# Performance work log

Hardware: AMD Instinct MI355X
Metric: run time of the kernel (lower is better)

Reference implementation:

```python
import jax, jax.numpy as jnp
import numpy as np

BS, S, D, H = 2, 2048, 1024, 16
DH = D // H  # 64


def setup_inputs() -> dict:
    key = jax.random.key(0)
    k1, k2, k3 = jax.random.split(key, 3)
    x = jax.random.normal(k1, (BS, S, D), dtype=jnp.float32)
    w_qkv = jax.random.normal(k2, (D, H, 3 * DH), dtype=jnp.float32) * (D ** -0.5)
    b_qkv = jnp.zeros((H, 3 * DH), dtype=jnp.float32)
    w_out = jax.random.normal(k3, (H, DH, D), dtype=jnp.float32) * (D ** -0.5)
    b_out = jnp.zeros((D,), dtype=jnp.float32)
    return {"x": x, "w_qkv": w_qkv, "b_qkv": b_qkv, "w_out": w_out, "b_out": b_out}


def reference(x, w_qkv, b_qkv, w_out, b_out):
    dtype = x.dtype
    # QKV projection: DenseGeneral(features=(H, 3*DH)) -> [B, S, H, 3*DH]
    qkv = jnp.einsum("bsd,dhf->bshf", x, w_qkv) + b_qkv
    q, k, v = jnp.split(qkv, 3, axis=-1)  # each [B, S, H, DH]

    scale = DH ** -0.5
    q = (q * scale).astype(jnp.float32)
    k = k.astype(jnp.float32)
    # Full causal attention with fp32 scores (as in original)
    weights = jnp.einsum("bqhd,bkhd->bhqk", q, k)  # [B, H, S, S]
    causal = jnp.tril(jnp.ones((S, S), dtype=bool))[None, None, :, :]
    weights = jnp.where(causal, weights, jnp.finfo(jnp.float32).min)
    weights = jax.nn.softmax(weights, axis=-1).astype(dtype)
    attn = jnp.einsum("bhqk,bkhd->bqhd", weights, v).astype(dtype)

    # Output projection: DenseGeneral(D, axis=(-2, -1))
    out = jnp.einsum("bqhd,hdo->bqo", attn, w_out) + b_out
    return out
```

## Files before the change

### kernel.cpp

```cpp
#include <hip/hip_runtime.h>
#include <hip/hip_bf16.h>
#include <stdint.h>

#define NBS 2
#define SEQ 2048
#define DMODEL 1024
#define NH 16
#define DHEAD 64
#define MROWS (NBS*SEQ)
#define NQKV (NH*3*DHEAD)

typedef __bf16 bf16;
typedef __bf16 bf16x8 __attribute__((ext_vector_type(8)));
typedef float f32x4 __attribute__((ext_vector_type(4)));

#define LOG2E 1.44269504088896f

static __device__ __forceinline__ void gload_lds16(const bf16* g, bf16* l) {
    __builtin_amdgcn_global_load_lds(
        (const __attribute__((address_space(1))) uint32_t*)g,
        (__attribute__((address_space(3))) uint32_t*)l, 16, 0, 0);
}

static __device__ __forceinline__ bf16x8 ld_b8(const bf16* p) {
    return __builtin_bit_cast(bf16x8, *(const uint4*)p);
}


__global__ void k_cvt(const float* __restrict__ in, bf16* __restrict__ out, int n4) {
    int i = blockIdx.x * blockDim.x + threadIdx.x;
    if (i < n4) {
        float4 v = ((const float4*)in)[i];
        ushort4 o;
        o.x = __builtin_bit_cast(unsigned short, (bf16)v.x);
        o.y = __builtin_bit_cast(unsigned short, (bf16)v.y);
        o.z = __builtin_bit_cast(unsigned short, (bf16)v.z);
        o.w = __builtin_bit_cast(unsigned short, (bf16)v.w);
        ((ushort4*)out)[i] = o;
    }
}

__global__ void k_tcvt(const float* __restrict__ in, bf16* __restrict__ out, int R, int C) {
    __shared__ float t[32][33];
    int tx = threadIdx.x, ty = threadIdx.y;
    int r0 = blockIdx.y * 32, c0 = blockIdx.x * 32;
#pragma unroll
    for (int i = 0; i < 4; i++)
        t[ty + i*8][tx] = in[(size_t)(r0 + ty + i*8) * C + (c0 + tx)];
    __syncthreads();
#pragma unroll
    for (int i = 0; i < 4; i++)
        out[(size_t)(c0 + ty + i*8) * R + (r0 + tx)] = (bf16)t[tx][ty + i*8];
}

template<int KD>
static __device__ __forceinline__ void gemm_tile(
        const bf16* __restrict__ A, const bf16* __restrict__ Bt,
        bf16* As, bf16* Bs, f32x4 acc[4][4], int tile_m, int tile_n) {
    int tid = threadIdx.x;
    int wave = tid >> 6, lane = tid & 63;
    int wr = wave >> 1, wc = wave & 1;
    int g = lane >> 4, r = lane & 15;
    int srow = lane >> 2, schunk = (lane & 3) * 8;

#pragma unroll
    for (int m = 0; m < 4; m++)
#pragma unroll
        for (int n = 0; n < 4; n++)
            acc[m][n] = (f32x4){0.f, 0.f, 0.f, 0.f};

    for (int k0 = 0; k0 < KD; k0 += 32) {
#pragma unroll
        for (int i = 0; i < 2; i++) {
            int ii = wave + i * 4;
            gload_lds16(A  + (size_t)(tile_m + ii*16 + srow) * KD + k0 + schunk, As + ii*512);
            gload_lds16(Bt + (size_t)(tile_n + ii*16 + srow) * KD + k0 + schunk, Bs + ii*512);
        }
        __syncthreads();
        bf16x8 af[4], bfr[4];
#pragma unroll
        for (int m = 0; m < 4; m++) af[m]  = *(const bf16x8*)(As + (wr*64 + m*16 + r)*32 + g*8);
#pragma unroll
        for (int n = 0; n < 4; n++) bfr[n] = *(const bf16x8*)(Bs + (wc*64 + n*16 + r)*32 + g*8);
#pragma unroll
        for (int m = 0; m < 4; m++)
#pragma unroll
            for (int n = 0; n < 4; n++)
                acc[m][n] = __builtin_amdgcn_mfma_f32_16x16x32_bf16(af[m], bfr[n], acc[m][n], 0, 0, 0);
        __syncthreads();
    }
}

__global__ __launch_bounds__(256) void k_gemm_qkv(
        const bf16* __restrict__ A, const bf16* __restrict__ Bt,
        const float* __restrict__ bias,
        bf16* __restrict__ Q, bf16* __restrict__ Kp, bf16* __restrict__ Vp) {
    __shared__ __align__(16) bf16 As[128*32];
    __shared__ __align__(16) bf16 Bs[128*32];
    f32x4 acc[4][4];
    int tile_m = blockIdx.y * 128, tile_n = blockIdx.x * 128;
    gemm_tile<DMODEL>(A, Bt, As, Bs, acc, tile_m, tile_n);

    int wave = threadIdx.x >> 6, lane = threadIdx.x & 63;
    int wr = wave >> 1, wc = wave & 1, g = lane >> 4, r = lane & 15;
#pragma unroll
    for (int m = 0; m < 4; m++) {
#pragma unroll
        for (int n = 0; n < 4; n++) {
            int col = tile_n + wc*64 + n*16 + r;
            int h = col / 192, f = col % 192;
            int kind = f >> 6, d = f & 63;
            float bv = bias[col];
#pragma unroll
            for (int j = 0; j < 4; j++) {
                int row = tile_m + wr*64 + m*16 + g*4 + j;
                int b = row >> 11, s = row & 2047;
                float v = acc[m][n][j] + bv;
                size_t addr = (((size_t)(b*NH + h)) * SEQ + s) * DHEAD + d;
                if (kind == 0)      Q[addr]  = (bf16)(v * 0.125f);
                else if (kind == 1) Kp[addr] = (bf16)v;
                else                Vp[addr] = (bf16)v;
            }
        }
    }
}

__global__ __launch_bounds__(256) void k_gemm_out(
        const bf16* __restrict__ A, const bf16* __restrict__ Bt,
        const float* __restrict__ bias, float* __restrict__ out) {
    __shared__ __align__(16) bf16 As[128*32];
    __shared__ __align__(16) bf16 Bs[128*32];
    f32x4 acc[4][4];
    int tile_m = blockIdx.y * 128, tile_n = blockIdx.x * 128;
    gemm_tile<DMODEL>(A, Bt, As, Bs, acc, tile_m, tile_n);

    int wave = threadIdx.x >> 6, lane = threadIdx.x & 63;
    int wr = wave >> 1, wc = wave & 1, g = lane >> 4, r = lane & 15;
#pragma unroll
    for (int m = 0; m < 4; m++) {
#pragma unroll
        for (int n = 0; n < 4; n++) {
            int col = tile_n + wc*64 + n*16 + r;
            float bv = bias[col];
#pragma unroll
            for (int j = 0; j < 4; j++) {
                int row = tile_m + wr*64 + m*16 + g*4 + j;
                out[(size_t)row * DMODEL + col] = acc[m][n][j] + bv;
            }
        }
    }
}

#define QBLK 128
#define KVB 64

__global__ __launch_bounds__(256) void k_attn(
        const bf16* __restrict__ Q, const bf16* __restrict__ K,
        const bf16* __restrict__ V, bf16* __restrict__ O) {
    int bh = blockIdx.y;
    int qc = (bh >= 16) ? (15 - blockIdx.x) : blockIdx.x;
    int q0 = qc * QBLK;
    int tid = threadIdx.x, wave = tid >> 6, lane = tid & 63;
    int g = lane >> 4, r = lane & 15;

    __shared__ __align__(16) bf16 Ks[2][KVB*72];
    __shared__ __align__(16) bf16 VsT[2][KVB*72];
    __shared__ __align__(16) bf16 Ps[4][32*72];

    const bf16* Kg = K + (size_t)bh * SEQ * DHEAD;
    const bf16* Vg = V + (size_t)bh * SEQ * DHEAD;

    bf16x8 qa[2][2];
#pragma unroll
    for (int mf = 0; mf < 2; mf++) {
        const bf16* qbase = Q + ((size_t)bh * SEQ + q0 + wave*32 + mf*16 + r) * DHEAD;
        qa[mf][0] = ld_b8(qbase + g*8);
        qa[mf][1] = ld_b8(qbase + 32 + g*8);
    }

    f32x4 o_acc[2][4];
    float l_sum[2][4];
#pragma unroll
    for (int mf = 0; mf < 2; mf++) {
#pragma unroll
        for (int t = 0; t < 4; t++) o_acc[mf][t] = (f32x4){0.f, 0.f, 0.f, 0.f};
#pragma unroll
        for (int j = 0; j < 4; j++) l_sum[mf][j] = 0.f;
    }

    int nt = 2*qc + 2;
    int qmax_wave = q0 + wave*32 + 31;

    int kc0 = tid, kc1 = tid + 256;
    int krow0 = kc0 >> 3, kseg0 = (kc0 & 7) * 8;
    int krow1 = kc1 >> 3, kseg1 = (kc1 & 7) * 8;
    int vrow = tid & 63, vd0 = (tid >> 6) * 8, vd1 = ((tid >> 6) + 4) * 8;

    bf16x8 kreg[2], vreg[2];
    kreg[0] = ld_b8(Kg + (size_t)krow0 * DHEAD + kseg0);
    kreg[1] = ld_b8(Kg + (size_t)krow1 * DHEAD + kseg1);
    vreg[0] = ld_b8(Vg + (size_t)vrow * DHEAD + vd0);
    vreg[1] = ld_b8(Vg + (size_t)vrow * DHEAD + vd1);

    int cur = 0;
    for (int t = 0; t < nt; t++) {
        int kv0 = t * KVB;
        *(uint4*)&Ks[cur][krow0*72 + kseg0] = __builtin_bit_cast(uint4, kreg[0]);
        *(uint4*)&Ks[cur][krow1*72 + kseg1] = __builtin_bit_cast(uint4, kreg[1]);
#pragma unroll
        for (int j = 0; j < 8; j++) VsT[cur][(vd0 + j)*72 + vrow] = vreg[0][j];
#pragma unroll
        for (int j = 0; j < 8; j++) VsT[cur][(vd1 + j)*72 + vrow] = vreg[1][j];
        __syncthreads();

        if (t + 1 < nt) {
            int kv1 = kv0 + KVB;
            kreg[0] = ld_b8(Kg + (size_t)(kv1 + krow0) * DHEAD + kseg0);
            kreg[1] = ld_b8(Kg + (size_t)(kv1 + krow1) * DHEAD + kseg1);
            vreg[0] = ld_b8(Vg + (size_t)(kv1 + vrow) * DHEAD + vd0);
            vreg[1] = ld_b8(Vg + (size_t)(kv1 + vrow) * DHEAD + vd1);
        }

        if (kv0 <= qmax_wave) {
#pragma unroll
            for (int mf = 0; mf < 2; mf++) {
                int qrow_min = q0 + wave*32 + mf*16;
                if (kv0 > qrow_min + 15) continue;
                f32x4 sc[4];
#pragma unroll
                for (int tt = 0; tt < 4; tt++) {
                    sc[tt] = (f32x4){0.f, 0.f, 0.f, 0.f};
#pragma unroll
                    for (int kk = 0; kk < 2; kk++) {
                        bf16x8 kb = ld_b8(&Ks[cur][(tt*16 + r)*72 + kk*32 + g*8]);
                        sc[tt] = __builtin_amdgcn_mfma_f32_16x16x32_bf16(qa[mf][kk], kb, sc[tt], 0, 0, 0);
                    }
                }
                bool need_mask = (kv0 + KVB - 1) > qrow_min;
#pragma unroll
                for (int tt = 0; tt < 4; tt++) {
#pragma unroll
                    for (int j = 0; j < 4; j++) {
                        float p = __builtin_amdgcn_exp2f(sc[tt][j] * LOG2E);
                        if (need_mask) {
                            int kcol = kv0 + tt*16 + r;
                            int qrow = qrow_min + g*4 + j;
                            if (kcol > qrow) p = 0.f;
                        }
                        l_sum[mf][j] += p;
                        Ps[wave][(mf*16 + g*4 + j)*72 + tt*16 + r] = (bf16)p;
                    }
                }
                bf16x8 pa[2];
#pragma unroll
                for (int kk = 0; kk < 2; kk++)
                    pa[kk] = ld_b8(&Ps[wave][(mf*16 + r)*72 + kk*32 + g*8]);
#pragma unroll
                for (int tt = 0; tt < 4; tt++) {
#pragma unroll
                    for (int kk = 0; kk < 2; kk++) {
                        bf16x8 vb = ld_b8(&VsT[cur][(tt*16 + r)*72 + kk*32 + g*8]);
                        o_acc[mf][tt] = __builtin_amdgcn_mfma_f32_16x16x32_bf16(pa[kk], vb, o_acc[mf][tt], 0, 0, 0);
                    }
                }
            }
        }
        cur ^= 1;
    }

#pragma unroll
    for (int mf = 0; mf < 2; mf++)
#pragma unroll
        for (int j = 0; j < 4; j++) {
            float s = l_sum[mf][j];
#pragma unroll
            for (int off = 1; off <= 8; off <<= 1) s += __shfl_xor(s, off);
            l_sum[mf][j] = 1.0f / s;
        }

    int b = bh >> 4, h = bh & 15;
#pragma unroll
    for (int mf = 0; mf < 2; mf++) {
#pragma unroll
        for (int t = 0; t < 4; t++) {
#pragma unroll
            for (int j = 0; j < 4; j++) {
                int qrow = q0 + wave*32 + mf*16 + g*4 + j;
                size_t addr = (((size_t)b * SEQ + qrow) * NH + h) * DHEAD + t*16 + r;
                O[addr] = (bf16)(o_acc[mf][t][j] * l_sum[mf][j]);
            }
        }
    }
}


extern "C" void kernel_launch(void* const* d_in, const int* in_sizes, int n_in,
                              void* d_out, int out_size, void* d_ws, size_t ws_size,
                              hipStream_t stream) {
    const float* x     = (const float*)d_in[0];
    const float* w_qkv = (const float*)d_in[1];
    const float* b_qkv = (const float*)d_in[2];
    const float* w_out = (const float*)d_in[3];
    const float* b_out = (const float*)d_in[4];
    float* out = (float*)d_out;

    char* ws = (char*)d_ws;
    bf16* xb   = (bf16*)(ws);
    bf16* wqkT = (bf16*)(ws + 8388608);
    bf16* woT  = (bf16*)(ws + 14680064);
    bf16* qb   = (bf16*)(ws + 16777216);
    bf16* kb   = (bf16*)(ws + 25165824);
    bf16* vb   = (bf16*)(ws + 33554432);
    bf16* attn = xb;

    k_cvt<<<(MROWS*DMODEL/4 + 255)/256, 256, 0, stream>>>(x, xb, MROWS*DMODEL/4);
    dim3 tb(32, 8);
    k_tcvt<<<dim3(NQKV/32, DMODEL/32), tb, 0, stream>>>(w_qkv, wqkT, DMODEL, NQKV);
    k_tcvt<<<dim3(DMODEL/32, DMODEL/32), tb, 0, stream>>>(w_out, woT, DMODEL, DMODEL);

    k_gemm_qkv<<<dim3(NQKV/128, MROWS/128), 256, 0, stream>>>(xb, wqkT, b_qkv, qb, kb, vb);
    k_attn<<<dim3(SEQ/QBLK, NBS*NH), 256, 0, stream>>>(qb, kb, vb, attn);
    k_gemm_out<<<dim3(DMODEL/128, MROWS/128), 256, 0, stream>>>(attn, woT, b_out, out);
}
```

Before: 134.7 us.

## Use 32x32x16 MFMA with transposed scores and register-resident P in attention

```diff
diff --git a/kernel.cpp b/kernel.cpp
--- a/kernel.cpp
+++ b/kernel.cpp
@@ -13,8 +13,11 @@
 typedef __bf16 bf16;
 typedef __bf16 bf16x8 __attribute__((ext_vector_type(8)));
 typedef float f32x4 __attribute__((ext_vector_type(4)));
+typedef float f32x16 __attribute__((ext_vector_type(16)));
+typedef unsigned int u32x2 __attribute__((ext_vector_type(2)));
 
 #define LOG2E 1.44269504088896f
+#define QSCALE (0.125f * LOG2E)
 
 static __device__ __forceinline__ void gload_lds16(const bf16* g, bf16* l) {
     __builtin_amdgcn_global_load_lds(
@@ -24,6 +27,24 @@
 
 static __device__ __forceinline__ bf16x8 ld_b8(const bf16* p) {
     return __builtin_bit_cast(bf16x8, *(const uint4*)p);
+}
+
+static __device__ __forceinline__ uint32_t pk_bf16(float lo, float hi) {
+    unsigned short l = __builtin_bit_cast(unsigned short, (bf16)lo);
+    unsigned short h = __builtin_bit_cast(unsigned short, (bf16)hi);
+    return ((uint32_t)h << 16) | (uint32_t)l;
+}
+
+static __device__ __forceinline__ u32x2 lane_swap32(uint32_t a, uint32_t b, int lane) {
+#if __has_builtin(__builtin_amdgcn_permlane32_swap)
+    return __builtin_amdgcn_permlane32_swap(a, b, false, false);
+#else
+    uint32_t sa = __shfl_xor(a, 32), sb = __shfl_xor(b, 32);
+    u32x2 r;
+    r.x = (lane >= 32) ? sb : a;
+    r.y = (lane >= 32) ? b : sa;
+    return r;
+#endif
 }
 
 
@@ -117,7 +138,7 @@
                 int b = row >> 11, s = row & 2047;
                 float v = acc[m][n][j] + bv;
                 size_t addr = (((size_t)(b*NH + h)) * SEQ + s) * DHEAD + d;
-                if (kind == 0)      Q[addr]  = (bf16)(v * 0.125f);
+                if (kind == 0)      Q[addr]  = (bf16)(v * QSCALE);
                 else if (kind == 1) Kp[addr] = (bf16)v;
                 else                Vp[addr] = (bf16)v;
             }
@@ -161,39 +182,31 @@
     int qc = (bh >= 16) ? (15 - blockIdx.x) : blockIdx.x;
     int q0 = qc * QBLK;
     int tid = threadIdx.x, wave = tid >> 6, lane = tid & 63;
-    int g = lane >> 4, r = lane & 15;
+    int l31 = lane & 31, hi = lane >> 5;
 
     __shared__ __align__(16) bf16 Ks[2][KVB*72];
     __shared__ __align__(16) bf16 VsT[2][KVB*72];
-    __shared__ __align__(16) bf16 Ps[4][32*72];
 
     const bf16* Kg = K + (size_t)bh * SEQ * DHEAD;
     const bf16* Vg = V + (size_t)bh * SEQ * DHEAD;
 
-    bf16x8 qa[2][2];
-#pragma unroll
-    for (int mf = 0; mf < 2; mf++) {
-        const bf16* qbase = Q + ((size_t)bh * SEQ + q0 + wave*32 + mf*16 + r) * DHEAD;
-        qa[mf][0] = ld_b8(qbase + g*8);
-        qa[mf][1] = ld_b8(qbase + 32 + g*8);
-    }
-
-    f32x4 o_acc[2][4];
-    float l_sum[2][4];
-#pragma unroll
-    for (int mf = 0; mf < 2; mf++) {
-#pragma unroll
-        for (int t = 0; t < 4; t++) o_acc[mf][t] = (f32x4){0.f, 0.f, 0.f, 0.f};
-#pragma unroll
-        for (int j = 0; j < 4; j++) l_sum[mf][j] = 0.f;
-    }
+    const bf16* qrow_p = Q + ((size_t)bh * SEQ + q0 + wave*32 + l31) * DHEAD;
+    bf16x8 qa2[4];
+#pragma unroll
+    for (int c = 0; c < 4; c++) qa2[c] = ld_b8(qrow_p + c*16 + hi*8);
+
+    f32x16 o32[2];
+    const f32x16 z16 = {0,0,0,0,0,0,0,0,0,0,0,0,0,0,0,0};
+    o32[0] = z16; o32[1] = z16;
+    float l_part = 0.f;
 
     int nt = 2*qc + 2;
+    int qrow = q0 + wave*32 + l31;
     int qmax_wave = q0 + wave*32 + 31;
-
-    int kc0 = tid, kc1 = tid + 256;
-    int krow0 = kc0 >> 3, kseg0 = (kc0 & 7) * 8;
-    int krow1 = kc1 >> 3, kseg1 = (kc1 & 7) * 8;
+    int qmin_wave = q0 + wave*32;
+
+    int krow0 = tid >> 3, kseg0 = (tid & 7) * 8;
+    int krow1 = (tid + 256) >> 3, kseg1 = (tid & 7) * 8;
     int vrow = tid & 63, vd0 = (tid >> 6) * 8, vd1 = ((tid >> 6) + 4) * 8;
 
     bf16x8 kreg[2], vreg[2];
@@ -222,74 +235,78 @@
         }
 
         if (kv0 <= qmax_wave) {
-#pragma unroll
-            for (int mf = 0; mf < 2; mf++) {
-                int qrow_min = q0 + wave*32 + mf*16;
-                if (kv0 > qrow_min + 15) continue;
-                f32x4 sc[4];
-#pragma unroll
-                for (int tt = 0; tt < 4; tt++) {
-                    sc[tt] = (f32x4){0.f, 0.f, 0.f, 0.f};
-#pragma unroll
-                    for (int kk = 0; kk < 2; kk++) {
-                        bf16x8 kb = ld_b8(&Ks[cur][(tt*16 + r)*72 + kk*32 + g*8]);
-                        sc[tt] = __builtin_amdgcn_mfma_f32_16x16x32_bf16(qa[mf][kk], kb, sc[tt], 0, 0, 0);
+            f32x16 st[2];
+            st[0] = z16; st[1] = z16;
+#pragma unroll
+            for (int c = 0; c < 4; c++) {
+#pragma unroll
+                for (int rb = 0; rb < 2; rb++) {
+                    bf16x8 kf = ld_b8(&Ks[cur][(rb*32 + l31)*72 + c*16 + hi*8]);
+                    st[rb] = __builtin_amdgcn_mfma_f32_32x32x16_bf16(kf, qa2[c], st[rb], 0, 0, 0);
+                }
+            }
+            bool needm = (kv0 + KVB - 1) > qmin_wave;
+            float l_add = 0.f;
+#pragma unroll
+            for (int rb = 0; rb < 2; rb++) {
+#pragma unroll
+                for (int reg = 0; reg < 16; reg++) {
+                    float e = __builtin_amdgcn_exp2f(st[rb][reg]);
+                    if (needm) {
+                        int kv = kv0 + rb*32 + (reg & 3) + 8*(reg >> 2) + 4*hi;
+                        if (kv > qrow) e = 0.f;
                     }
+                    l_add += e;
+                    st[rb][reg] = e;
                 }
-                bool need_mask = (kv0 + KVB - 1) > qrow_min;
-#pragma unroll
-                for (int tt = 0; tt < 4; tt++) {
-#pragma unroll
-                    for (int j = 0; j < 4; j++) {
-                        float p = __builtin_amdgcn_exp2f(sc[tt][j] * LOG2E);
-                        if (need_mask) {
-                            int kcol = kv0 + tt*16 + r;
-                            int qrow = qrow_min + g*4 + j;
-                            if (kcol > qrow) p = 0.f;
-                        }
-                        l_sum[mf][j] += p;
-                        Ps[wave][(mf*16 + g*4 + j)*72 + tt*16 + r] = (bf16)p;
-                    }
+            }
+            l_part += l_add;
+
+            bf16x8 pa[4];
+#pragma unroll
+            for (int c = 0; c < 4; c++) {
+                const f32x16& pp = st[c >> 1];
+                const int base = (c & 1) * 8;
+                uint32_t a0 = pk_bf16(pp[base+0], pp[base+1]);
+                uint32_t a1 = pk_bf16(pp[base+2], pp[base+3]);
+                uint32_t b0 = pk_bf16(pp[base+4], pp[base+5]);
+                uint32_t b1 = pk_bf16(pp[base+6], pp[base+7]);
+                u32x2 s0 = lane_swap32(a0, b0, lane);
+                u32x2 s1 = lane_swap32(a1, b1, lane);
+                uint4 fr = {s0.x, s1.x, s0.y, s1.y};
+                pa[c] = __builtin_bit_cast(bf16x8, fr);
+            }
+
+#pragma unroll
+            for (int dblk = 0; dblk < 2; dblk++) {
+#pragma unroll
+                for (int c = 0; c < 4; c++) {
+                    bf16x8 vf = ld_b8(&VsT[cur][(dblk*32 + l31)*72 + c*16 + hi*8]);
+                    o32[dblk] = __builtin_amdgcn_mfma_f32_32x32x16_bf16(pa[c], vf, o32[dblk], 0, 0, 0);
                 }
-                bf16x8 pa[2];
-#pragma unroll
-                for (int kk = 0; kk < 2; kk++)
-                    pa[kk] = ld_b8(&Ps[wave][(mf*16 + r)*72 + kk*32 + g*8]);
-#pragma unroll
-                for (int tt = 0; tt < 4; tt++) {
-#pragma unroll
-                    for (int kk = 0; kk < 2; kk++) {
-                        bf16x8 vb = ld_b8(&VsT[cur][(tt*16 + r)*72 + kk*32 + g*8]);
-                        o_acc[mf][tt] = __builtin_amdgcn_mfma_f32_16x16x32_bf16(pa[kk], vb, o_acc[mf][tt], 0, 0, 0);
-                    }
-                }
             }
         }
         cur ^= 1;
     }
 
-#pragma unroll
-    for (int mf = 0; mf < 2; mf++)
-#pragma unroll
-        for (int j = 0; j < 4; j++) {
-            float s = l_sum[mf][j];
-#pragma unroll
-            for (int off = 1; off <= 8; off <<= 1) s += __shfl_xor(s, off);
-            l_sum[mf][j] = 1.0f / s;
-        }
+    l_part += __shfl_xor(l_part, 32);
+    float linv = 1.0f / l_part;
+
+    float lrv[16];
+#pragma unroll
+    for (int reg = 0; reg < 16; reg++) {
+        int qr = (reg & 3) + 8*(reg >> 2) + 4*hi;
+        lrv[reg] = __shfl(linv, qr);
+    }
 
     int b = bh >> 4, h = bh & 15;
 #pragma unroll
-    for (int mf = 0; mf < 2; mf++) {
-#pragma unroll
-        for (int t = 0; t < 4; t++) {
-#pragma unroll
-            for (int j = 0; j < 4; j++) {
-                int qrow = q0 + wave*32 + mf*16 + g*4 + j;
-                size_t addr = (((size_t)b * SEQ + qrow) * NH + h) * DHEAD + t*16 + r;
-                O[addr] = (bf16)(o_acc[mf][t][j] * l_sum[mf][j]);
-            }
-        }
+    for (int reg = 0; reg < 16; reg++) {
+        int qr = (reg & 3) + 8*(reg >> 2) + 4*hi;
+        int srow = q0 + wave*32 + qr;
+        size_t base = (((size_t)b * SEQ + srow) * NH + h) * DHEAD + l31;
+        O[base]      = (bf16)(o32[0][reg] * lrv[reg]);
+        O[base + 32] = (bf16)(o32[1][reg] * lrv[reg]);
     }
 }
 
```

Result: faster. 124.7 us (-7.5%).
